# Kernel tuning notes

Hardware: AMD Instinct MI355X
Metric: run time of the kernel (lower is better)

Reference implementation:

```python
import jax, jax.numpy as jnp
import numpy as np

NH = 16  # num_heads from init_kwargs


def setup_inputs() -> dict:
    key = jax.random.key(0)
    ks = jax.random.split(key, 7)
    B, L, S, H = 4, 2, 1024, 1024
    s = 0.02  # weight init scale to keep logits numerically tame
    return {
        "x": jax.random.normal(ks[0], (B, S, H), jnp.float32),
        "y": jax.random.normal(ks[1], (L, B, S, H), jnp.float32),
        "bias": jax.random.normal(ks[2], (B, 1, 1, S), jnp.float32),
        "Wq": jax.random.normal(ks[3], (H, H), jnp.float32) * s,
        "Wk": jax.random.normal(ks[4], (L, H, H), jnp.float32) * s,
        "Wv": jax.random.normal(ks[5], (L, H, H), jnp.float32) * s,
        "Wo": jax.random.normal(ks[6], (H, H), jnp.float32) * s,
    }


def reference(x, y, bias, Wq, Wk, Wv, Wo):
    # x: [B, Lq, H]; y: [L, B, Lk, H] (stacked list of per-link memories)
    B, Lq, H = x.shape
    L, _, Lk, _ = y.shape
    d = H // NH

    # shared query projection, split heads: [B, NH, Lq, d], pre-scaled
    q = (x @ Wq).reshape(B, Lq, NH, d).transpose(0, 2, 1, 3) * (d ** -0.5)

    # per-link K/V projections, split heads -> [B, L, NH, Lk, d]
    kp = jnp.einsum('lbsh,lhe->lbse', y, Wk).reshape(L, B, Lk, NH, d).transpose(1, 0, 3, 2, 4)
    vp = jnp.einsum('lbsh,lhe->lbse', y, Wv).reshape(L, B, Lk, NH, d).transpose(1, 0, 3, 2, 4)

    # per-link logits [B, L, NH, Lq, Lk] + broadcast bias (concat across links == broadcast)
    logits = jnp.einsum('bhqd,blhkd->blhqk', q, kp) + bias[:, None]

    # computation_mode == 1: joint softmax over the link-summed logits
    joint = logits.sum(axis=1)                # [B, NH, Lq, Lk]
    w = jax.nn.softmax(joint, axis=-1)        # (training=False -> no dropout)

    # sum_l (w @ v_l) == w @ sum_l v_l  (w is shared across links)
    ctx = jnp.einsum('bhqk,bhkd->bhqd', w, vp.sum(axis=1))

    # combine heads [B, Lq, H] and output projection
    out = ctx.transpose(0, 2, 1, 3).reshape(B, Lq, H) @ Wo
    return out
```

## Files before the change

kernel.cpp:

```cpp
#include <hip/hip_runtime.h>
#include <cstdint>

typedef __bf16 bf16_t;
typedef bf16_t bf16x4 __attribute__((ext_vector_type(4)));
typedef bf16_t bf16x8 __attribute__((ext_vector_type(8)));
typedef float f32x4 __attribute__((ext_vector_type(4)));

#define GLD_LDS16(g, l)                                                        \
  __builtin_amdgcn_global_load_lds(                                            \
      (const __attribute__((address_space(1))) void*)(g),                      \
      (__attribute__((address_space(3))) void*)(l), 16, 0, 0)

#define LOG2E 1.44269504088896340736f

static __device__ __forceinline__ unsigned short bf16_bits(float f) {
  bf16_t h = (bf16_t)f;
  return __builtin_bit_cast(unsigned short, h);
}

__global__ void prep_kernel(const float* __restrict__ x,
                            const float* __restrict__ y,
                            const float* __restrict__ Wq,
                            const float* __restrict__ Wk,
                            const float* __restrict__ Wv,
                            const float* __restrict__ Wo,
                            bf16_t* __restrict__ xb, bf16_t* __restrict__ yb,
                            bf16_t* __restrict__ WqT,
                            bf16_t* __restrict__ WkvT,
                            bf16_t* __restrict__ WoT) {
  __shared__ float tile[32][33];
  int bid = blockIdx.x;
  if (bid < 6144) {
    int i = bid * 256 + threadIdx.x;
    const float* src;
    bf16_t* dst;
    if (i < 524288) { src = x; dst = xb; }
    else            { src = y; dst = yb; i -= 524288; }
    const float4* s = (const float4*)src;
    float4 a = s[i * 2];
    float4 b = s[i * 2 + 1];
    bf16x8 o;
    o[0] = (bf16_t)a.x; o[1] = (bf16_t)a.y; o[2] = (bf16_t)a.z; o[3] = (bf16_t)a.w;
    o[4] = (bf16_t)b.x; o[5] = (bf16_t)b.y; o[6] = (bf16_t)b.z; o[7] = (bf16_t)b.w;
    *(bf16x8*)(dst + (size_t)i * 8) = o;
    return;
  }
  bid -= 6144;
  const float* src; bf16_t* dst; int R, lb;
  if (bid < 1024)      { src = Wq; dst = WqT;                        R = 1024; lb = bid; }
  else if (bid < 3072) { src = Wk; dst = WkvT;                       R = 2048; lb = bid - 1024; }
  else if (bid < 5120) { src = Wv; dst = WkvT + (size_t)1024 * 2048; R = 2048; lb = bid - 3072; }
  else                 { src = Wo; dst = WoT;                        R = 1024; lb = bid - 5120; }
  int c0 = (lb & 31) << 5, r0 = (lb >> 5) << 5;
  int tc = threadIdx.x & 31, tr = threadIdx.x >> 5;
#pragma unroll
  for (int i = 0; i < 4; i++)
    tile[tr + i * 8][tc] = src[(size_t)(r0 + tr + i * 8) * 1024 + c0 + tc];
  __syncthreads();
#pragma unroll
  for (int i = 0; i < 4; i++)
    dst[(size_t)(c0 + tr + i * 8) * R + r0 + tc] = (bf16_t)tile[tc][tr + i * 8];
}

template <int MODE>
__global__ __launch_bounds__(256, 2) void gemm_bt(
    const bf16_t* __restrict__ A0, const bf16_t* __restrict__ A1, int lda,
    int Ksplit, const bf16_t* __restrict__ BT, int Ktot,
    void* __restrict__ Cp, void* __restrict__ Cp2, int ldc, float scale) {
  __shared__ bf16_t As[2][128 * 32];
  __shared__ bf16_t Bs[2][128 * 32];
  const int t = threadIdx.x, w = t >> 6, l = t & 63;
  const int l15 = l & 15, l4 = l >> 4;
  const int wr = w >> 1, wc = w & 1;
  const int i = blockIdx.x;
  const int yb = (i & 7) * 4 + ((i >> 3) & 3);
  const int xb = i >> 5;
  const int m0 = yb * 128, n0 = xb * 128;
  f32x4 acc[4][4] = {};
  const int nkt = Ktot >> 5;
  const int c0 = t, c1 = t + 256;
  const int ar0 = c0 >> 2, ak0 = (c0 & 3) * 8;
  const int ar1 = c1 >> 2, ak1 = (c1 & 3) * 8;

#define GEMM_STAGE(buf, kt)                                                    \
  {                                                                            \
    const int kbase = (kt) * 32;                                               \
    int kg0 = kbase + ak0;                                                     \
    const bf16_t* s0 = (kg0 < Ksplit)                                          \
                           ? (A0 + (size_t)(m0 + ar0) * lda + kg0)             \
                           : (A1 + (size_t)(m0 + ar0) * lda + (kg0 - Ksplit)); \
    GLD_LDS16(s0, As[buf] + c0 * 8);                                           \
    int kg1 = kbase + ak1;                                                     \
    const bf16_t* s1 = (kg1 < Ksplit)                                          \
                           ? (A0 + (size_t)(m0 + ar1) * lda + kg1)             \
                           : (A1 + (size_t)(m0 + ar1) * lda + (kg1 - Ksplit)); \
    GLD_LDS16(s1, As[buf] + c1 * 8);                                           \
    const bf16_t* b0 = BT + (size_t)(n0 + ar0) * Ktot + kbase + ak0;           \
    GLD_LDS16(b0, Bs[buf] + c0 * 8);                                           \
    const bf16_t* b1 = BT + (size_t)(n0 + ar1) * Ktot + kbase + ak1;           \
    GLD_LDS16(b1, Bs[buf] + c1 * 8);                                           \
  }

  GEMM_STAGE(0, 0);
  __syncthreads();
  int cur = 0;
  for (int kt = 0; kt < nkt; ++kt) {
    if (kt + 1 < nkt) GEMM_STAGE(cur ^ 1, kt + 1);
    bf16x8 af[4], bfr[4];
#pragma unroll
    for (int mi = 0; mi < 4; mi++)
      af[mi] = *(const bf16x8*)&As[cur][(wr * 64 + mi * 16 + l15) * 32 + l4 * 8];
#pragma unroll
    for (int ni = 0; ni < 4; ni++)
      bfr[ni] = *(const bf16x8*)&Bs[cur][(wc * 64 + ni * 16 + l15) * 32 + l4 * 8];
#pragma unroll
    for (int mi = 0; mi < 4; mi++)
#pragma unroll
      for (int ni = 0; ni < 4; ni++)
        acc[mi][ni] = __builtin_amdgcn_mfma_f32_16x16x32_bf16(
            af[mi], bfr[ni], acc[mi][ni], 0, 0, 0);
    __syncthreads();
    cur ^= 1;
  }

#pragma unroll
  for (int mi = 0; mi < 4; mi++) {
#pragma unroll
    for (int ni = 0; ni < 4; ni++) {
      const int rbase = m0 + wr * 64 + mi * 16 + l4 * 4;
      const int col = n0 + wc * 64 + ni * 16 + l15;
      if (MODE == 0) {
        bf16_t* C = (bf16_t*)Cp;
#pragma unroll
        for (int rr = 0; rr < 4; rr++)
          C[(size_t)(rbase + rr) * ldc + col] =
              (bf16_t)(acc[mi][ni][rr] * scale);
      } else if (MODE == 2) {
        float* C = (float*)Cp;
#pragma unroll
        for (int rr = 0; rr < 4; rr++)
          C[(size_t)(rbase + rr) * ldc + col] = acc[mi][ni][rr];
      } else {
        if (n0 < 1024) {
          bf16_t* C = (bf16_t*)Cp;
#pragma unroll
          for (int rr = 0; rr < 4; rr++)
            C[(size_t)(rbase + rr) * ldc + col] = (bf16_t)acc[mi][ni][rr];
        } else {
          bf16_t* VT = (bf16_t*)Cp2;
          union { unsigned short u[4]; uint2 v; } pk;
#pragma unroll
          for (int rr = 0; rr < 4; rr++)
            pk.u[rr] = bf16_bits(acc[mi][ni][rr]);
          *(uint2*)&VT[(size_t)(col - 1024) * 4096 + rbase] = pk.v;
        }
      }
    }
  }
#undef GEMM_STAGE
}

__global__ __launch_bounds__(256, 4) void attn_kernel(
    const bf16_t* __restrict__ Q, const bf16_t* __restrict__ K,
    const bf16_t* __restrict__ VT, const float* __restrict__ bias,
    bf16_t* __restrict__ ctx) {
  __shared__ bf16_t Ks[2][64 * 64];
  __shared__ bf16_t Vs[2][64 * 64];
  __shared__ bf16_t Ps[4][1024];
  const int t = threadIdx.x, w = t >> 6, l = t & 63;
  const int l15 = l & 15, l4 = l >> 4;
  const int id = blockIdx.x;
  const int bh = id & 63, qt = id >> 6;
  const int b = bh >> 4, h = bh & 15;

  bf16x8 qf[2];
  {
    const bf16_t* Qb =
        Q + (size_t)(b * 1024 + qt * 64 + w * 16 + l15) * 1024 + h * 64;
#pragma unroll
    for (int ks = 0; ks < 2; ks++)
      qf[ks] = *(const bf16x8*)&Qb[ks * 32 + l4 * 8];
  }

#define ATTN_STAGE(buf, kt)                                                    \
  {                                                                            \
    _Pragma("unroll") for (int j = 0; j < 2; j++) {                            \
      int c = t + j * 256;                                                     \
      int row = c >> 3, sl = (c & 7) ^ (row & 7);                              \
      const bf16_t* srck =                                                     \
          K + (size_t)(b * 1024 + (kt) * 64 + row) * 1024 + h * 64 + sl * 8;   \
      GLD_LDS16(srck, Ks[buf] + c * 8);                                        \
      const bf16_t* srcv =                                                     \
          VT + (size_t)(h * 64 + row) * 4096 + b * 1024 + (kt) * 64 + sl * 8;  \
      GLD_LDS16(srcv, Vs[buf] + c * 8);                                        \
    }                                                                          \
  }

  float mrun = -INFINITY, lrun = 0.f;
  f32x4 ctxacc[4] = {};

  ATTN_STAGE(0, 0);
  __syncthreads();
  int cur = 0;
  for (int kt = 0; kt < 16; ++kt) {
    if (kt + 1 < 16) ATTN_STAGE(cur ^ 1, kt + 1);

    f32x4 sacc[4] = {};
#pragma unroll
    for (int ks = 0; ks < 2; ks++) {
#pragma unroll
      for (int ni = 0; ni < 4; ni++) {
        int krow = ni * 16 + l15;
        int eoff = (krow * 64 + ks * 32 + l4 * 8) ^ ((krow & 7) << 3);
        bf16x8 kf = *(const bf16x8*)&Ks[cur][eoff];
        sacc[ni] = __builtin_amdgcn_mfma_f32_16x16x32_bf16(kf, qf[ks],
                                                           sacc[ni], 0, 0, 0);
      }
    }
#pragma unroll
    for (int ni = 0; ni < 4; ni++) {
      float4 bb =
          *(const float4*)&bias[b * 1024 + kt * 64 + ni * 16 + l4 * 4];
      sacc[ni][0] += (2.0f * LOG2E) * bb.x;
      sacc[ni][1] += (2.0f * LOG2E) * bb.y;
      sacc[ni][2] += (2.0f * LOG2E) * bb.z;
      sacc[ni][3] += (2.0f * LOG2E) * bb.w;
    }
    float tm = -INFINITY;
#pragma unroll
    for (int ni = 0; ni < 4; ni++)
#pragma unroll
      for (int rr = 0; rr < 4; rr++) tm = fmaxf(tm, sacc[ni][rr]);
    tm = fmaxf(tm, __shfl_xor(tm, 16));
    tm = fmaxf(tm, __shfl_xor(tm, 32));
    float mnew = fmaxf(mrun, tm);
    float sc = exp2f(mrun - mnew);
    float rsum = 0.f;
#pragma unroll
    for (int ni = 0; ni < 4; ni++) {
      bf16x4 pk;
#pragma unroll
      for (int rr = 0; rr < 4; rr++) {
        float p = exp2f(sacc[ni][rr] - mnew);
        rsum += p;
        pk[rr] = (bf16_t)p;
      }
      *(bf16x4*)&Ps[w][(ni * 2 + (l4 >> 1)) * 128 + l15 * 8 + (l4 & 1) * 4] =
          pk;
    }
    rsum += __shfl_xor(rsum, 16);
    rsum += __shfl_xor(rsum, 32);
    lrun = lrun * sc + rsum;
    mrun = mnew;
#pragma unroll
    for (int ni = 0; ni < 4; ni++) ctxacc[ni] *= sc;
#pragma unroll
    for (int kk = 0; kk < 2; kk++) {
      bf16x8 pf = *(const bf16x8*)&Ps[w][(kk * 4 + l4) * 128 + l15 * 8];
#pragma unroll
      for (int ni = 0; ni < 4; ni++) {
        int drow = ni * 16 + l15;
        int voff = (drow * 64 + kk * 32 + l4 * 8) ^ ((drow & 7) << 3);
        bf16x8 vf = *(const bf16x8*)&Vs[cur][voff];
        ctxacc[ni] = __builtin_amdgcn_mfma_f32_16x16x32_bf16(vf, pf, ctxacc[ni],
                                                             0, 0, 0);
      }
    }
    __syncthreads();
    cur ^= 1;
  }

  bf16_t* T = Ks[0];
  {
    float inv = 1.0f / lrun;
    int q = w * 16 + l15;
#pragma unroll
    for (int ni = 0; ni < 4; ni++) {
      bf16x4 tv;
#pragma unroll
      for (int rr = 0; rr < 4; rr++) tv[rr] = (bf16_t)(ctxacc[ni][rr] * inv);
      int d0 = ni * 16 + l4 * 4;
      *(bf16x4*)&T[q * 64 + (d0 ^ ((l15 & 7) << 3))] = tv;
    }
  }
  __syncthreads();
#pragma unroll
  for (int c = t; c < 512; c += 256) {
    int row = c >> 3, col8 = c & 7;
    bf16x8 v = *(const bf16x8*)&T[row * 64 + ((col8 * 8) ^ ((row & 7) << 3))];
    *(bf16x8*)&ctx[(size_t)(b * 1024 + qt * 64 + row) * 1024 + h * 64 +
                   col8 * 8] = v;
  }
#undef ATTN_STAGE
}

extern "C" void kernel_launch(void* const* d_in, const int* in_sizes, int n_in,
                              void* d_out, int out_size, void* d_ws,
                              size_t ws_size, hipStream_t stream) {
  const float* x = (const float*)d_in[0];
  const float* y = (const float*)d_in[1];
  const float* bias = (const float*)d_in[2];
  const float* Wq = (const float*)d_in[3];
  const float* Wk = (const float*)d_in[4];
  const float* Wv = (const float*)d_in[5];
  const float* Wo = (const float*)d_in[6];
  float* out = (float*)d_out;

  char* ws = (char*)d_ws;
  const size_t MB = 1024 * 1024;
  bf16_t* xb   = (bf16_t*)(ws + 0 * MB);
  bf16_t* yb   = (bf16_t*)(ws + 8 * MB);
  bf16_t* WqT  = (bf16_t*)(ws + 24 * MB);
  bf16_t* WkvT = (bf16_t*)(ws + 26 * MB);
  bf16_t* WoT  = (bf16_t*)(ws + 34 * MB);
  bf16_t* Qb   = (bf16_t*)(ws + 36 * MB);
  bf16_t* Kb   = (bf16_t*)(ws + 44 * MB);
  bf16_t* VTb  = (bf16_t*)(ws + 52 * MB);
  bf16_t* ctxb = (bf16_t*)(ws + 60 * MB);

  prep_kernel<<<12288, 256, 0, stream>>>(x, y, Wq, Wk, Wv, Wo, xb, yb, WqT,
                                         WkvT, WoT);

  gemm_bt<0><<<256, 256, 0, stream>>>(xb, xb, 1024, 1024, WqT, 1024, Qb,
                                      nullptr, 1024, 0.125f * LOG2E);
  gemm_bt<3><<<512, 256, 0, stream>>>(yb, yb + (size_t)4096 * 1024, 1024, 1024,
                                      WkvT, 2048, Kb, VTb, 1024, 1.0f);
  attn_kernel<<<1024, 256, 0, stream>>>(Qb, Kb, VTb, bias, ctxb);
  gemm_bt<2><<<256, 256, 0, stream>>>(ctxb, ctxb, 1024, 1024, WoT, 1024, out,
                                      nullptr, 1024, 1.0f);
}
```

Baseline: 157.7 us.

## Merge Q and KV projection GEMMs into one launch and swizzle LDS tiles

Replaces the templated GEMM with a combined QKV kernel that handles the Q projection and the stacked K/V projection in a single 768-block grid, plus a dedicated output-projection kernel. Adds an XOR swizzle on the LDS column chunk, applied on both the async global-to-LDS writes and the fragment reads, to cut bank conflicts. Strides are hardcoded to 1024. This removes one kernel launch and its tail, but mixes blocks with different K lengths in one grid, which can unbalance scheduling.

```diff
diff --git a/kernel.cpp b/kernel.cpp
--- a/kernel.cpp
+++ b/kernel.cpp
@@ -62,38 +62,19 @@
     dst[(size_t)(c0 + tr + i * 8) * R + r0 + tc] = (bf16_t)tile[tc][tr + i * 8];
 }
 
-template <int MODE>
-__global__ __launch_bounds__(256, 2) void gemm_bt(
-    const bf16_t* __restrict__ A0, const bf16_t* __restrict__ A1, int lda,
-    int Ksplit, const bf16_t* __restrict__ BT, int Ktot,
-    void* __restrict__ Cp, void* __restrict__ Cp2, int ldc, float scale) {
-  __shared__ bf16_t As[2][128 * 32];
-  __shared__ bf16_t Bs[2][128 * 32];
-  const int t = threadIdx.x, w = t >> 6, l = t & 63;
-  const int l15 = l & 15, l4 = l >> 4;
-  const int wr = w >> 1, wc = w & 1;
-  const int i = blockIdx.x;
-  const int yb = (i & 7) * 4 + ((i >> 3) & 3);
-  const int xb = i >> 5;
-  const int m0 = yb * 128, n0 = xb * 128;
-  f32x4 acc[4][4] = {};
-  const int nkt = Ktot >> 5;
-  const int c0 = t, c1 = t + 256;
-  const int ar0 = c0 >> 2, ak0 = (c0 & 3) * 8;
-  const int ar1 = c1 >> 2, ak1 = (c1 & 3) * 8;
 
 #define GEMM_STAGE(buf, kt)                                                    \
   {                                                                            \
     const int kbase = (kt) * 32;                                               \
     int kg0 = kbase + ak0;                                                     \
     const bf16_t* s0 = (kg0 < Ksplit)                                          \
-                           ? (A0 + (size_t)(m0 + ar0) * lda + kg0)             \
-                           : (A1 + (size_t)(m0 + ar0) * lda + (kg0 - Ksplit)); \
+                           ? (A0 + (size_t)(m0 + ar0) * 1024 + kg0)            \
+                           : (A1 + (size_t)(m0 + ar0) * 1024 + (kg0 - Ksplit));\
     GLD_LDS16(s0, As[buf] + c0 * 8);                                           \
     int kg1 = kbase + ak1;                                                     \
     const bf16_t* s1 = (kg1 < Ksplit)                                          \
-                           ? (A0 + (size_t)(m0 + ar1) * lda + kg1)             \
-                           : (A1 + (size_t)(m0 + ar1) * lda + (kg1 - Ksplit)); \
+                           ? (A0 + (size_t)(m0 + ar1) * 1024 + kg1)            \
+                           : (A1 + (size_t)(m0 + ar1) * 1024 + (kg1 - Ksplit));\
     GLD_LDS16(s1, As[buf] + c1 * 8);                                           \
     const bf16_t* b0 = BT + (size_t)(n0 + ar0) * Ktot + kbase + ak0;           \
     GLD_LDS16(b0, Bs[buf] + c0 * 8);                                           \
@@ -101,27 +82,63 @@
     GLD_LDS16(b1, Bs[buf] + c1 * 8);                                           \
   }
 
-  GEMM_STAGE(0, 0);
-  __syncthreads();
-  int cur = 0;
-  for (int kt = 0; kt < nkt; ++kt) {
-    if (kt + 1 < nkt) GEMM_STAGE(cur ^ 1, kt + 1);
-    bf16x8 af[4], bfr[4];
-#pragma unroll
-    for (int mi = 0; mi < 4; mi++)
-      af[mi] = *(const bf16x8*)&As[cur][(wr * 64 + mi * 16 + l15) * 32 + l4 * 8];
-#pragma unroll
-    for (int ni = 0; ni < 4; ni++)
-      bfr[ni] = *(const bf16x8*)&Bs[cur][(wc * 64 + ni * 16 + l15) * 32 + l4 * 8];
-#pragma unroll
-    for (int mi = 0; mi < 4; mi++)
-#pragma unroll
-      for (int ni = 0; ni < 4; ni++)
-        acc[mi][ni] = __builtin_amdgcn_mfma_f32_16x16x32_bf16(
-            af[mi], bfr[ni], acc[mi][ni], 0, 0, 0);
-    __syncthreads();
-    cur ^= 1;
-  }
+#define GEMM_DECLS                                                             \
+  const int t = threadIdx.x, w = t >> 6, l = t & 63;                           \
+  const int l15 = l & 15, l4 = l >> 4;                                         \
+  const int wr = w >> 1, wc = w & 1;                                           \
+  const int c0 = t, c1 = t + 256;                                              \
+  const int ar0 = c0 >> 2, ar1 = c1 >> 2;                                      \
+  const int ak0 = ((c0 & 3) ^ ((ar0 >> 1) & 3)) * 8;                           \
+  const int ak1 = ((c1 & 3) ^ ((ar1 >> 1) & 3)) * 8;                           \
+  int offA[4], offB[4];                                                        \
+  _Pragma("unroll") for (int mi = 0; mi < 4; mi++) {                           \
+    int rA = wr * 64 + mi * 16 + l15;                                          \
+    offA[mi] = rA * 32 + (l4 ^ ((rA >> 1) & 3)) * 8;                           \
+    int rB = wc * 64 + mi * 16 + l15;                                          \
+    offB[mi] = rB * 32 + (l4 ^ ((rB >> 1) & 3)) * 8;                           \
+  }
+
+#define GEMM_MAINLOOP                                                          \
+  GEMM_STAGE(0, 0);                                                            \
+  __syncthreads();                                                             \
+  int cur = 0;                                                                 \
+  for (int kt = 0; kt < nkt; ++kt) {                                           \
+    if (kt + 1 < nkt) GEMM_STAGE(cur ^ 1, kt + 1);                             \
+    bf16x8 af[4], bfr[4];                                                      \
+    _Pragma("unroll") for (int mi = 0; mi < 4; mi++)                           \
+        af[mi] = *(const bf16x8*)&As[cur][offA[mi]];                           \
+    _Pragma("unroll") for (int ni = 0; ni < 4; ni++)                           \
+        bfr[ni] = *(const bf16x8*)&Bs[cur][offB[ni]];                          \
+    _Pragma("unroll") for (int mi = 0; mi < 4; mi++)                           \
+        _Pragma("unroll") for (int ni = 0; ni < 4; ni++)                       \
+            acc[mi][ni] = __builtin_amdgcn_mfma_f32_16x16x32_bf16(             \
+                af[mi], bfr[ni], acc[mi][ni], 0, 0, 0);                        \
+    __syncthreads();                                                           \
+    cur ^= 1;                                                                  \
+  }
+
+__global__ __launch_bounds__(256, 2) void qkv_kernel(
+    const bf16_t* __restrict__ xbp, const bf16_t* __restrict__ ybp,
+    const bf16_t* __restrict__ WqT, const bf16_t* __restrict__ WkvT,
+    bf16_t* __restrict__ Qb, bf16_t* __restrict__ Kb,
+    bf16_t* __restrict__ VTb) {
+  __shared__ bf16_t As[2][128 * 32];
+  __shared__ bf16_t Bs[2][128 * 32];
+  GEMM_DECLS
+  const bool isQ = blockIdx.x < 256;
+  const int i = isQ ? blockIdx.x : blockIdx.x - 256;
+  const int ybt = (i & 7) * 4 + ((i >> 3) & 3);
+  const int xbt = i >> 5;
+  const int m0 = ybt * 128, n0 = xbt * 128;
+  const bf16_t* A0 = isQ ? xbp : ybp;
+  const bf16_t* A1 = isQ ? xbp : ybp + (size_t)4096 * 1024;
+  const int Ksplit = 1024;
+  const bf16_t* BT = isQ ? WqT : WkvT;
+  const int Ktot = isQ ? 1024 : 2048;
+  const int nkt = Ktot >> 5;
+  f32x4 acc[4][4] = {};
+
+  GEMM_MAINLOOP
 
 #pragma unroll
   for (int mi = 0; mi < 4; mi++) {
@@ -129,35 +146,53 @@
     for (int ni = 0; ni < 4; ni++) {
       const int rbase = m0 + wr * 64 + mi * 16 + l4 * 4;
       const int col = n0 + wc * 64 + ni * 16 + l15;
-      if (MODE == 0) {
-        bf16_t* C = (bf16_t*)Cp;
+      if (isQ) {
 #pragma unroll
         for (int rr = 0; rr < 4; rr++)
-          C[(size_t)(rbase + rr) * ldc + col] =
-              (bf16_t)(acc[mi][ni][rr] * scale);
-      } else if (MODE == 2) {
-        float* C = (float*)Cp;
+          Qb[(size_t)(rbase + rr) * 1024 + col] =
+              (bf16_t)(acc[mi][ni][rr] * (0.125f * LOG2E));
+      } else if (n0 < 1024) {
 #pragma unroll
         for (int rr = 0; rr < 4; rr++)
-          C[(size_t)(rbase + rr) * ldc + col] = acc[mi][ni][rr];
+          Kb[(size_t)(rbase + rr) * 1024 + col] = (bf16_t)acc[mi][ni][rr];
       } else {
-        if (n0 < 1024) {
-          bf16_t* C = (bf16_t*)Cp;
-#pragma unroll
-          for (int rr = 0; rr < 4; rr++)
-            C[(size_t)(rbase + rr) * ldc + col] = (bf16_t)acc[mi][ni][rr];
-        } else {
-          bf16_t* VT = (bf16_t*)Cp2;
-          union { unsigned short u[4]; uint2 v; } pk;
-#pragma unroll
-          for (int rr = 0; rr < 4; rr++)
-            pk.u[rr] = bf16_bits(acc[mi][ni][rr]);
-          *(uint2*)&VT[(size_t)(col - 1024) * 4096 + rbase] = pk.v;
-        }
+        union { unsigned short u[4]; uint2 v; } pk;
+#pragma unroll
+        for (int rr = 0; rr < 4; rr++)
+          pk.u[rr] = bf16_bits(acc[mi][ni][rr]);
+        *(uint2*)&VTb[(size_t)(col - 1024) * 4096 + rbase] = pk.v;
       }
     }
   }
-#undef GEMM_STAGE
+}
+
+__global__ __launch_bounds__(256, 2) void gemm_o(const bf16_t* __restrict__ A0,
+                                                 const bf16_t* __restrict__ BT,
+                                                 float* __restrict__ Cp) {
+  __shared__ bf16_t As[2][128 * 32];
+  __shared__ bf16_t Bs[2][128 * 32];
+  GEMM_DECLS
+  const int i = blockIdx.x;
+  const int ybt = (i & 7) * 4 + ((i >> 3) & 3);
+  const int xbt = i >> 5;
+  const int m0 = ybt * 128, n0 = xbt * 128;
+  const bf16_t* A1 = A0;
+  const int Ksplit = 1024, Ktot = 1024, nkt = 32;
+  f32x4 acc[4][4] = {};
+
+  GEMM_MAINLOOP
+
+#pragma unroll
+  for (int mi = 0; mi < 4; mi++) {
+#pragma unroll
+    for (int ni = 0; ni < 4; ni++) {
+      const int rbase = m0 + wr * 64 + mi * 16 + l4 * 4;
+      const int col = n0 + wc * 64 + ni * 16 + l15;
+#pragma unroll
+      for (int rr = 0; rr < 4; rr++)
+        Cp[(size_t)(rbase + rr) * 1024 + col] = acc[mi][ni][rr];
+    }
+  }
 }
 
 __global__ __launch_bounds__(256, 4) void attn_kernel(
@@ -320,12 +355,7 @@
 
   prep_kernel<<<12288, 256, 0, stream>>>(x, y, Wq, Wk, Wv, Wo, xb, yb, WqT,
                                          WkvT, WoT);
-
-  gemm_bt<0><<<256, 256, 0, stream>>>(xb, xb, 1024, 1024, WqT, 1024, Qb,
-                                      nullptr, 1024, 0.125f * LOG2E);
-  gemm_bt<3><<<512, 256, 0, stream>>>(yb, yb + (size_t)4096 * 1024, 1024, 1024,
-                                      WkvT, 2048, Kb, VTb, 1024, 1.0f);
+  qkv_kernel<<<768, 256, 0, stream>>>(xb, yb, WqT, WkvT, Qb, Kb, VTb);
   attn_kernel<<<1024, 256, 0, stream>>>(Qb, Kb, VTb, bias, ctxb);
-  gemm_bt<2><<<256, 256, 0, stream>>>(ctxb, ctxb, 1024, 1024, WoT, 1024, out,
-                                      nullptr, 1024, 1.0f);
-}
+  gemm_o<<<256, 256, 0, stream>>>(ctxb, WoT, out);
+}
```

After: 137.8 us. 12.6% less time.

## Merge Q and KV projections into one 256x256-tile triple-buffered GEMM launch

Applied to the files above, without the earlier changes.

Replaces the separate Q and K/V projection GEMMs with a single 512-thread kernel. It uses 256x256 output tiles, a three-stage LDS pipeline with explicit vmcnt waits, split-phase loads and s_setprio around the MFMA bursts. Both this kernel and the output-projection GEMM gain an XOR swizzle on LDS layout to reduce bank conflicts. The merge removes one launch and raises per-block data reuse, but the grid drops to 192 blocks, which may leave CUs underfilled. The larger accumulator count also raises register pressure.

```diff
diff --git a/kernel.cpp b/kernel.cpp
--- a/kernel.cpp
+++ b/kernel.cpp
@@ -12,6 +12,14 @@
       (__attribute__((address_space(3))) void*)(l), 16, 0, 0)
 
 #define LOG2E 1.44269504088896340736f
+#define SBAR() __builtin_amdgcn_sched_barrier(0)
+
+static __device__ __forceinline__ void wait_vm4() {
+  asm volatile("s_waitcnt vmcnt(4)" ::: "memory");
+}
+static __device__ __forceinline__ void wait_vm0() {
+  asm volatile("s_waitcnt vmcnt(0)" ::: "memory");
+}
 
 static __device__ __forceinline__ unsigned short bf16_bits(float f) {
   bf16_t h = (bf16_t)f;
@@ -62,57 +70,193 @@
     dst[(size_t)(c0 + tr + i * 8) * R + r0 + tc] = (bf16_t)tile[tc][tr + i * 8];
 }
 
-template <int MODE>
-__global__ __launch_bounds__(256, 2) void gemm_bt(
-    const bf16_t* __restrict__ A0, const bf16_t* __restrict__ A1, int lda,
-    int Ksplit, const bf16_t* __restrict__ BT, int Ktot,
-    void* __restrict__ Cp, void* __restrict__ Cp2, int ldc, float scale) {
+__global__ __launch_bounds__(512, 2) void qkv_kernel(
+    const bf16_t* __restrict__ xbp, const bf16_t* __restrict__ ybp,
+    const bf16_t* __restrict__ WqT, const bf16_t* __restrict__ WkvT,
+    bf16_t* __restrict__ Qb, bf16_t* __restrict__ Kb,
+    bf16_t* __restrict__ VTb) {
+  __shared__ bf16_t As[3][256 * 32];
+  __shared__ bf16_t Bs[3][256 * 32];
+  const int t = threadIdx.x, w = t >> 6, l = t & 63;
+  const int l15 = l & 15, l4 = l >> 4;
+  const int wr = w >> 2, wc = w & 3;
+  const bool isQ = blockIdx.x < 64;
+  const int i = isQ ? blockIdx.x : blockIdx.x - 64;
+  const int ybt = (i & 7) * 2 + ((i >> 3) & 1);
+  const int xbt = i >> 4;
+  const int m0 = ybt * 256, n0 = xbt * 256;
+  const bf16_t* A0 = isQ ? xbp : ybp;
+  const bf16_t* A1 = isQ ? xbp : ybp + (size_t)4096 * 1024;
+  const int Ksplit = 1024;
+  const bf16_t* BT = isQ ? WqT : WkvT;
+  const int Ktot = isQ ? 1024 : 2048;
+  const int nkt = Ktot >> 5;
+
+  f32x4 acc[8][4] = {};
+
+  int offA[8], offB[4];
+#pragma unroll
+  for (int mi = 0; mi < 8; mi++) {
+    int row = wr * 128 + mi * 16 + l15;
+    offA[mi] = row * 32 + (l4 ^ ((row >> 1) & 3)) * 8;
+  }
+#pragma unroll
+  for (int ni = 0; ni < 4; ni++) {
+    int row = wc * 64 + ni * 16 + l15;
+    offB[ni] = row * 32 + (l4 ^ ((row >> 1) & 3)) * 8;
+  }
+
+#define ST_A(buf, kt)                                                          \
+  {                                                                            \
+    const int kbase = (kt) * 32;                                               \
+    _Pragma("unroll") for (int j = 0; j < 2; j++) {                            \
+      int c = (j * 8 + w) * 64 + l;                                            \
+      int row = c >> 2;                                                        \
+      int ks = ((c & 3) ^ ((row >> 1) & 3)) * 8;                               \
+      int kg = kbase + ks;                                                     \
+      const bf16_t* s = (kg < Ksplit)                                          \
+                            ? (A0 + (size_t)(m0 + row) * 1024 + kg)            \
+                            : (A1 + (size_t)(m0 + row) * 1024 + (kg - Ksplit));\
+      GLD_LDS16(s, As[buf] + c * 8);                                           \
+    }                                                                          \
+  }
+#define ST_B(buf, kt)                                                          \
+  {                                                                            \
+    const int kbase = (kt) * 32;                                               \
+    _Pragma("unroll") for (int j = 0; j < 2; j++) {                            \
+      int c = (j * 8 + w) * 64 + l;                                            \
+      int row = c >> 2;                                                        \
+      int ks = ((c & 3) ^ ((row >> 1) & 3)) * 8;                               \
+      const bf16_t* s = BT + (size_t)(n0 + row) * Ktot + kbase + ks;           \
+      GLD_LDS16(s, Bs[buf] + c * 8);                                           \
+    }                                                                          \
+  }
+
+  ST_A(0, 0); ST_B(0, 0);
+  ST_A(1, 1); ST_B(1, 1);
+  wait_vm4();
+  SBAR();
+  __builtin_amdgcn_s_barrier();
+
+  int cur = 0;
+  for (int kt = 0; kt < nkt; ++kt) {
+    int nx2 = cur + 2; if (nx2 >= 3) nx2 -= 3;
+    const bool more = (kt + 2 < nkt);
+    bf16x8 bfr[4], af[4];
+    if (more) ST_A(nx2, kt + 2);
+#pragma unroll
+    for (int ni = 0; ni < 4; ni++)
+      bfr[ni] = *(const bf16x8*)&Bs[cur][offB[ni]];
+#pragma unroll
+    for (int mi = 0; mi < 4; mi++)
+      af[mi] = *(const bf16x8*)&As[cur][offA[mi]];
+    __builtin_amdgcn_s_setprio(1);
+#pragma unroll
+    for (int mi = 0; mi < 4; mi++)
+#pragma unroll
+      for (int ni = 0; ni < 4; ni++)
+        acc[mi][ni] = __builtin_amdgcn_mfma_f32_16x16x32_bf16(
+            af[mi], bfr[ni], acc[mi][ni], 0, 0, 0);
+    __builtin_amdgcn_s_setprio(0);
+    __builtin_amdgcn_s_barrier();
+    if (more) ST_B(nx2, kt + 2);
+#pragma unroll
+    for (int mi = 0; mi < 4; mi++)
+      af[mi] = *(const bf16x8*)&As[cur][offA[mi + 4]];
+    __builtin_amdgcn_s_setprio(1);
+#pragma unroll
+    for (int mi = 0; mi < 4; mi++)
+#pragma unroll
+      for (int ni = 0; ni < 4; ni++)
+        acc[mi + 4][ni] = __builtin_amdgcn_mfma_f32_16x16x32_bf16(
+            af[mi], bfr[ni], acc[mi + 4][ni], 0, 0, 0);
+    __builtin_amdgcn_s_setprio(0);
+    if (more) wait_vm4(); else wait_vm0();
+    SBAR();
+    __builtin_amdgcn_s_barrier();
+    cur = (cur == 2) ? 0 : cur + 1;
+  }
+#undef ST_A
+#undef ST_B
+
+#pragma unroll
+  for (int mi = 0; mi < 8; mi++) {
+#pragma unroll
+    for (int ni = 0; ni < 4; ni++) {
+      const int rbase = m0 + wr * 128 + mi * 16 + l4 * 4;
+      const int col = n0 + wc * 64 + ni * 16 + l15;
+      if (isQ) {
+#pragma unroll
+        for (int rr = 0; rr < 4; rr++)
+          Qb[(size_t)(rbase + rr) * 1024 + col] =
+              (bf16_t)(acc[mi][ni][rr] * (0.125f * LOG2E));
+      } else if (n0 < 1024) {
+#pragma unroll
+        for (int rr = 0; rr < 4; rr++)
+          Kb[(size_t)(rbase + rr) * 1024 + col] = (bf16_t)acc[mi][ni][rr];
+      } else {
+        union { unsigned short u[4]; uint2 v; } pk;
+#pragma unroll
+        for (int rr = 0; rr < 4; rr++)
+          pk.u[rr] = bf16_bits(acc[mi][ni][rr]);
+        *(uint2*)&VTb[(size_t)(col - 1024) * 4096 + rbase] = pk.v;
+      }
+    }
+  }
+}
+
+__global__ __launch_bounds__(256, 2) void gemm_o(const bf16_t* __restrict__ A0,
+                                                 const bf16_t* __restrict__ BT,
+                                                 float* __restrict__ Cp) {
   __shared__ bf16_t As[2][128 * 32];
   __shared__ bf16_t Bs[2][128 * 32];
   const int t = threadIdx.x, w = t >> 6, l = t & 63;
   const int l15 = l & 15, l4 = l >> 4;
   const int wr = w >> 1, wc = w & 1;
+  const int c0 = t, c1 = t + 256;
+  const int ar0 = c0 >> 2, ar1 = c1 >> 2;
+  const int ak0 = ((c0 & 3) ^ ((ar0 >> 1) & 3)) * 8;
+  const int ak1 = ((c1 & 3) ^ ((ar1 >> 1) & 3)) * 8;
+  int offA[4], offB[4];
+#pragma unroll
+  for (int mi = 0; mi < 4; mi++) {
+    int rA = wr * 64 + mi * 16 + l15;
+    offA[mi] = rA * 32 + (l4 ^ ((rA >> 1) & 3)) * 8;
+    int rB = wc * 64 + mi * 16 + l15;
+    offB[mi] = rB * 32 + (l4 ^ ((rB >> 1) & 3)) * 8;
+  }
   const int i = blockIdx.x;
-  const int yb = (i & 7) * 4 + ((i >> 3) & 3);
-  const int xb = i >> 5;
-  const int m0 = yb * 128, n0 = xb * 128;
+  const int ybt = (i & 7) * 4 + ((i >> 3) & 3);
+  const int xbt = i >> 5;
+  const int m0 = ybt * 128, n0 = xbt * 128;
+  const int nkt = 32;
   f32x4 acc[4][4] = {};
-  const int nkt = Ktot >> 5;
-  const int c0 = t, c1 = t + 256;
-  const int ar0 = c0 >> 2, ak0 = (c0 & 3) * 8;
-  const int ar1 = c1 >> 2, ak1 = (c1 & 3) * 8;
-
-#define GEMM_STAGE(buf, kt)                                                    \
+
+#define OST(buf, kt)                                                           \
   {                                                                            \
     const int kbase = (kt) * 32;                                               \
-    int kg0 = kbase + ak0;                                                     \
-    const bf16_t* s0 = (kg0 < Ksplit)                                          \
-                           ? (A0 + (size_t)(m0 + ar0) * lda + kg0)             \
-                           : (A1 + (size_t)(m0 + ar0) * lda + (kg0 - Ksplit)); \
+    const bf16_t* s0 = A0 + (size_t)(m0 + ar0) * 1024 + kbase + ak0;           \
     GLD_LDS16(s0, As[buf] + c0 * 8);                                           \
-    int kg1 = kbase + ak1;                                                     \
-    const bf16_t* s1 = (kg1 < Ksplit)                                          \
-                           ? (A0 + (size_t)(m0 + ar1) * lda + kg1)             \
-                           : (A1 + (size_t)(m0 + ar1) * lda + (kg1 - Ksplit)); \
+    const bf16_t* s1 = A0 + (size_t)(m0 + ar1) * 1024 + kbase + ak1;           \
     GLD_LDS16(s1, As[buf] + c1 * 8);                                           \
-    const bf16_t* b0 = BT + (size_t)(n0 + ar0) * Ktot + kbase + ak0;           \
+    const bf16_t* b0 = BT + (size_t)(n0 + ar0) * 1024 + kbase + ak0;           \
     GLD_LDS16(b0, Bs[buf] + c0 * 8);                                           \
-    const bf16_t* b1 = BT + (size_t)(n0 + ar1) * Ktot + kbase + ak1;           \
+    const bf16_t* b1 = BT + (size_t)(n0 + ar1) * 1024 + kbase + ak1;           \
     GLD_LDS16(b1, Bs[buf] + c1 * 8);                                           \
   }
 
-  GEMM_STAGE(0, 0);
+  OST(0, 0);
   __syncthreads();
   int cur = 0;
   for (int kt = 0; kt < nkt; ++kt) {
-    if (kt + 1 < nkt) GEMM_STAGE(cur ^ 1, kt + 1);
+    if (kt + 1 < nkt) OST(cur ^ 1, kt + 1);
     bf16x8 af[4], bfr[4];
 #pragma unroll
     for (int mi = 0; mi < 4; mi++)
-      af[mi] = *(const bf16x8*)&As[cur][(wr * 64 + mi * 16 + l15) * 32 + l4 * 8];
+      af[mi] = *(const bf16x8*)&As[cur][offA[mi]];
 #pragma unroll
     for (int ni = 0; ni < 4; ni++)
-      bfr[ni] = *(const bf16x8*)&Bs[cur][(wc * 64 + ni * 16 + l15) * 32 + l4 * 8];
+      bfr[ni] = *(const bf16x8*)&Bs[cur][offB[ni]];
 #pragma unroll
     for (int mi = 0; mi < 4; mi++)
 #pragma unroll
@@ -122,6 +266,7 @@
     __syncthreads();
     cur ^= 1;
   }
+#undef OST
 
 #pragma unroll
   for (int mi = 0; mi < 4; mi++) {
@@ -129,35 +274,11 @@
     for (int ni = 0; ni < 4; ni++) {
       const int rbase = m0 + wr * 64 + mi * 16 + l4 * 4;
       const int col = n0 + wc * 64 + ni * 16 + l15;
-      if (MODE == 0) {
-        bf16_t* C = (bf16_t*)Cp;
-#pragma unroll
-        for (int rr = 0; rr < 4; rr++)
-          C[(size_t)(rbase + rr) * ldc + col] =
-              (bf16_t)(acc[mi][ni][rr] * scale);
-      } else if (MODE == 2) {
-        float* C = (float*)Cp;
-#pragma unroll
-        for (int rr = 0; rr < 4; rr++)
-          C[(size_t)(rbase + rr) * ldc + col] = acc[mi][ni][rr];
-      } else {
-        if (n0 < 1024) {
-          bf16_t* C = (bf16_t*)Cp;
-#pragma unroll
-          for (int rr = 0; rr < 4; rr++)
-            C[(size_t)(rbase + rr) * ldc + col] = (bf16_t)acc[mi][ni][rr];
-        } else {
-          bf16_t* VT = (bf16_t*)Cp2;
-          union { unsigned short u[4]; uint2 v; } pk;
-#pragma unroll
-          for (int rr = 0; rr < 4; rr++)
-            pk.u[rr] = bf16_bits(acc[mi][ni][rr]);
-          *(uint2*)&VT[(size_t)(col - 1024) * 4096 + rbase] = pk.v;
-        }
-      }
-    }
-  }
-#undef GEMM_STAGE
+#pragma unroll
+      for (int rr = 0; rr < 4; rr++)
+        Cp[(size_t)(rbase + rr) * 1024 + col] = acc[mi][ni][rr];
+    }
+  }
 }
 
 __global__ __launch_bounds__(256, 4) void attn_kernel(
@@ -320,12 +441,7 @@
 
   prep_kernel<<<12288, 256, 0, stream>>>(x, y, Wq, Wk, Wv, Wo, xb, yb, WqT,
                                          WkvT, WoT);
-
-  gemm_bt<0><<<256, 256, 0, stream>>>(xb, xb, 1024, 1024, WqT, 1024, Qb,
-                                      nullptr, 1024, 0.125f * LOG2E);
-  gemm_bt<3><<<512, 256, 0, stream>>>(yb, yb + (size_t)4096 * 1024, 1024, 1024,
-                                      WkvT, 2048, Kb, VTb, 1024, 1.0f);
+  qkv_kernel<<<192, 512, 0, stream>>>(xb, yb, WqT, WkvT, Qb, Kb, VTb);
   attn_kernel<<<1024, 256, 0, stream>>>(Qb, Kb, VTb, bias, ctxb);
-  gemm_bt<2><<<256, 256, 0, stream>>>(ctxb, ctxb, 1024, 1024, WoT, 1024, out,
-                                      nullptr, 1024, 1.0f);
-}
+  gemm_o<<<256, 256, 0, stream>>>(ctxb, WoT, out);
+}
```

New measurement: 162.3 us. 1.03x slower.
